# Optimization experiments

Hardware: AMD Instinct MI355X
Metric: run time of the kernel (lower is better)

The kernel has to match this reference:

```python
import jax, jax.numpy as jnp
import numpy as np

T, H, I, E, TOPK = 8192, 2048, 4096, 8, 2

def setup_inputs() -> dict:
    key = jax.random.key(0)
    k1, k2, k3, k4 = jax.random.split(key, 4)
    x = jax.random.normal(k1, (T, H), dtype=jnp.float32)
    gate_w = jax.random.normal(k2, (E, H), dtype=jnp.float32) * 0.02
    ws = jax.random.normal(k3, (E, 2 * I, H), dtype=jnp.float32) * 0.02
    w2s = jax.random.normal(k4, (E, H, I), dtype=jnp.float32) * 0.02
    return {"x": x, "gate_w": gate_w, "ws": ws, "w2s": w2s, "top_k": TOPK}

def reference(x, gate_w, ws, w2s, top_k):
    num_tokens = x.shape[0]
    num_experts = ws.shape[0]
    inter = w2s.shape[2]
    # --- router (fused_topk): softmax -> top-k -> renormalize ---
    logits = x @ gate_w.T                       # [T, E]
    probs = jax.nn.softmax(logits, axis=-1)
    topk_w, topk_ids = jax.lax.top_k(probs, top_k)   # [T, K]
    if top_k > 1:
        topk_w = topk_w / jnp.sum(topk_w, axis=-1, keepdims=True)
    # dense combine-weights [E, T]: sum of routing weights per (token, expert)
    tok = jnp.arange(num_tokens)
    cw = jnp.zeros((num_tokens, num_experts), dtype=x.dtype)
    cw = cw.at[tok[:, None], topk_ids].add(topk_w)
    cw = cw.T                                   # [E, T]
    # --- fused_experts: per-expert gated-SiLU MLP, weighted combine ---
    def body(acc, inp):
        e_ws, e_w2, e_cw = inp                  # [2I,H], [H,I], [T]
        gu = x @ e_ws.T                         # [T, 2I]
        g, u = gu[:, :inter], gu[:, inter:]
        h = jax.nn.silu(g) * u                  # SiluAndMul
        out = h @ e_w2.T                        # [T, H]
        return acc + e_cw[:, None] * out, None
    init = jnp.zeros_like(x)
    final, _ = jax.lax.scan(body, init, (ws, w2s, cw))
    return final
```

## Files before the change

### kernel.cpp

```cpp
#include <hip/hip_runtime.h>
#include <hip/hip_fp16.h>
#include <cstdint>
#include <cstddef>

#define TTOK 8192
#define HD   2048
#define ID   4096
#define NE   8
#define NPAIR (TTOK * 2)
#define PADMAX (NPAIR + NE * 128)

typedef _Float16 h8 __attribute__((ext_vector_type(8)));
typedef _Float16 h4 __attribute__((ext_vector_type(4)));
typedef float    f4 __attribute__((ext_vector_type(4)));

__device__ __forceinline__ void async_cp16(const void* g, void* l) {
  __builtin_amdgcn_global_load_lds(
      (const __attribute__((address_space(1))) unsigned int*)g,
      (__attribute__((address_space(3))) unsigned int*)l, 16, 0, 0);
}

__device__ __forceinline__ f4 zero4() { f4 z = {0.f, 0.f, 0.f, 0.f}; return z; }

__global__ void cvt_kernel(const float* __restrict__ src, _Float16* __restrict__ dst, size_t n) {
  size_t stride = (size_t)gridDim.x * blockDim.x * 8;
  for (size_t i = ((size_t)blockIdx.x * blockDim.x + threadIdx.x) * 8; i < n; i += stride) {
    const float4* s = (const float4*)(src + i);
    float4 a = s[0], b = s[1];
    h8 o;
    o[0] = (_Float16)a.x; o[1] = (_Float16)a.y; o[2] = (_Float16)a.z; o[3] = (_Float16)a.w;
    o[4] = (_Float16)b.x; o[5] = (_Float16)b.y; o[6] = (_Float16)b.z; o[7] = (_Float16)b.w;
    *(h8*)(dst + i) = o;
  }
}

__global__ __launch_bounds__(256) void gate_kernel(
    const float* __restrict__ x, const float* __restrict__ gw,
    int* __restrict__ counts, int* __restrict__ tids, float* __restrict__ tw) {
  int lane = threadIdx.x & 63;
  int t = blockIdx.x * 4 + (threadIdx.x >> 6);
  const float* xr = x + (size_t)t * HD;
  float acc[NE];
#pragma unroll
  for (int e = 0; e < NE; e++) acc[e] = 0.f;
  for (int j = lane; j < HD; j += 64) {
    float xv = xr[j];
#pragma unroll
    for (int e = 0; e < NE; e++) acc[e] += xv * gw[e * HD + j];
  }
#pragma unroll
  for (int off = 32; off > 0; off >>= 1) {
#pragma unroll
    for (int e = 0; e < NE; e++) acc[e] += __shfl_xor(acc[e], off, 64);
  }
  if (lane == 0) {
    int e0 = 0; float v0 = acc[0];
#pragma unroll
    for (int e = 1; e < NE; e++) if (acc[e] > v0) { v0 = acc[e]; e0 = e; }
    int e1 = -1; float v1 = -1e30f;
#pragma unroll
    for (int e = 0; e < NE; e++) if (e != e0 && acc[e] > v1) { v1 = acc[e]; e1 = e; }
    float b = __expf(v1 - v0);
    float w0 = 1.f / (1.f + b);
    tids[2 * t] = e0; tids[2 * t + 1] = e1;
    tw[2 * t] = w0;   tw[2 * t + 1] = b * w0;
    atomicAdd(&counts[e0], 1); atomicAdd(&counts[e1], 1);
  }
}

__global__ void scan_kernel(const int* __restrict__ counts, int* __restrict__ offs,
                            int* __restrict__ cursor) {
  if (threadIdx.x == 0 && blockIdx.x == 0) {
    int off = 0;
    for (int e = 0; e < NE; e++) {
      offs[e] = off; cursor[e] = off;
      off += ((counts[e] + 127) >> 7) << 7;
    }
    offs[NE] = off;
  }
}

__global__ void scatter_kernel(const int* __restrict__ tids, const float* __restrict__ tw,
                               int* __restrict__ cursor, int* __restrict__ perm,
                               float* __restrict__ pw) {
  int t = blockIdx.x * 256 + threadIdx.x;
#pragma unroll
  for (int k = 0; k < 2; k++) {
    int e = tids[2 * t + k];
    int pos = atomicAdd(&cursor[e], 1);
    perm[pos] = t; pw[pos] = tw[2 * t + k];
  }
}

__global__ void padfill_kernel(const int* __restrict__ counts, const int* __restrict__ offs,
                               int* __restrict__ perm) {
  int s = blockIdx.x * 256 + threadIdx.x;
#pragma unroll
  for (int e = 0; e < NE; e++) {
    if (s >= offs[e] + counts[e] && s < offs[e + 1]) perm[s] = -1;
  }
}

template <bool WPRE>
__global__ __launch_bounds__(256, 2) void gemm1_kernel(
    const _Float16* __restrict__ xh, const float* __restrict__ wsf,
    const _Float16* __restrict__ wsh,
    const int* __restrict__ counts, const int* __restrict__ offs,
    const int* __restrict__ perm, _Float16* __restrict__ hbuf) {
  int e = blockIdx.y >> 6, rb = blockIdx.y & 63;
  if (rb >= ((counts[e] + 127) >> 7)) return;
  int row0 = offs[e] + (rb << 7);
  int n0 = blockIdx.x << 7;

  __shared__ _Float16 As[128 * 32];
  __shared__ _Float16 Bg[128 * 32];
  __shared__ _Float16 Bu[128 * 32];
  int tid = threadIdx.x, lane = tid & 63, wid = tid >> 6, wr = wid >> 1, wc = wid & 1;

  const _Float16* asrc[2];
#pragma unroll
  for (int i = 0; i < 2; i++) {
    int slot = i * 256 + tid, r = slot >> 2, seg = slot & 3;
    int p = perm[row0 + r]; if (p < 0) p = 0;
    asrc[i] = xh + (size_t)p * HD + seg * 8;
  }
  const _Float16* bsg[2]; const _Float16* bsu[2];
  const float* fsg = nullptr; const float* fsu = nullptr;
  if constexpr (WPRE) {
#pragma unroll
    for (int i = 0; i < 2; i++) {
      int slot = i * 256 + tid, r = slot >> 2, seg = slot & 3;
      bsg[i] = wsh + ((size_t)e * 2 * ID + n0 + r) * HD + seg * 8;
      bsu[i] = wsh + ((size_t)e * 2 * ID + ID + n0 + r) * HD + seg * 8;
    }
  } else {
    int tr = tid >> 1, hf = tid & 1;
    fsg = wsf + ((size_t)e * 2 * ID + n0 + tr) * HD + hf * 16;
    fsu = wsf + ((size_t)e * 2 * ID + ID + n0 + tr) * HD + hf * 16;
  }

  auto stage = [&](int kt) {
    int kof = kt * 32;
#pragma unroll
    for (int i = 0; i < 2; i++) async_cp16(asrc[i] + kof, &As[(i * 256 + tid) * 8]);
    if constexpr (WPRE) {
#pragma unroll
      for (int i = 0; i < 2; i++) {
        async_cp16(bsg[i] + kof, &Bg[(i * 256 + tid) * 8]);
        async_cp16(bsu[i] + kof, &Bu[(i * 256 + tid) * 8]);
      }
    } else {
      int tr = tid >> 1, hf = tid & 1;
#pragma unroll
      for (int j = 0; j < 4; j++) {
        float4 vg = *(const float4*)(fsg + kof + j * 4);
        float4 vu = *(const float4*)(fsu + kof + j * 4);
        h4 og, ou;
        og[0] = (_Float16)vg.x; og[1] = (_Float16)vg.y; og[2] = (_Float16)vg.z; og[3] = (_Float16)vg.w;
        ou[0] = (_Float16)vu.x; ou[1] = (_Float16)vu.y; ou[2] = (_Float16)vu.z; ou[3] = (_Float16)vu.w;
        *(h4*)&Bg[tr * 32 + hf * 16 + j * 4] = og;
        *(h4*)&Bu[tr * 32 + hf * 16 + j * 4] = ou;
      }
    }
  };

  f4 accg[4][4], accu[4][4];
#pragma unroll
  for (int m = 0; m < 4; m++)
#pragma unroll
    for (int n = 0; n < 4; n++) { accg[m][n] = zero4(); accu[m][n] = zero4(); }

  stage(0);
  const int NK = HD / 32;
  for (int kt = 0; kt < NK; ++kt) {
    __syncthreads();
    int lr = lane & 15, ks = lane >> 4;
    h8 af[4], bg[4], bu[4];
#pragma unroll
    for (int m = 0; m < 4; m++)
      af[m] = *(const h8*)&As[((wr << 6) + (m << 4) + lr) * 32 + ks * 8];
#pragma unroll
    for (int n = 0; n < 4; n++) {
      bg[n] = *(const h8*)&Bg[((wc << 6) + (n << 4) + lr) * 32 + ks * 8];
      bu[n] = *(const h8*)&Bu[((wc << 6) + (n << 4) + lr) * 32 + ks * 8];
    }
#pragma unroll
    for (int m = 0; m < 4; m++)
#pragma unroll
      for (int n = 0; n < 4; n++) {
        accg[m][n] = __builtin_amdgcn_mfma_f32_16x16x32_f16(af[m], bg[n], accg[m][n], 0, 0, 0);
        accu[m][n] = __builtin_amdgcn_mfma_f32_16x16x32_f16(af[m], bu[n], accu[m][n], 0, 0, 0);
      }
    __syncthreads();
    if (kt + 1 < NK) stage(kt + 1);
  }

  int lr = lane & 15, lg = lane >> 4;
#pragma unroll
  for (int m = 0; m < 4; m++)
#pragma unroll
    for (int n = 0; n < 4; n++)
#pragma unroll
      for (int r = 0; r < 4; r++) {
        int grow = (wr << 6) + (m << 4) + (lg << 2) + r;
        int gcol = n0 + (wc << 6) + (n << 4) + lr;
        float g = accg[m][n][r], u = accu[m][n][r];
        float hv = g / (1.f + __expf(-g)) * u;
        hbuf[(size_t)(row0 + grow) * ID + gcol] = (_Float16)hv;
      }
}

template <bool WPRE>
__global__ __launch_bounds__(256, 2) void gemm2_kernel(
    const _Float16* __restrict__ hbuf, const float* __restrict__ w2f,
    const _Float16* __restrict__ w2h,
    const int* __restrict__ counts, const int* __restrict__ offs,
    const int* __restrict__ perm, const float* __restrict__ pw,
    float* __restrict__ out) {
  int e = blockIdx.y >> 6, rb = blockIdx.y & 63;
  if (rb >= ((counts[e] + 127) >> 7)) return;
  int row0 = offs[e] + (rb << 7);
  int n0 = blockIdx.x << 7;

  __shared__ _Float16 As[128 * 32];
  __shared__ _Float16 Bs[128 * 32];
  int tid = threadIdx.x, lane = tid & 63, wid = tid >> 6, wr = wid >> 1, wc = wid & 1;

  const _Float16* asrc[2]; const _Float16* bs[2]; const float* fs = nullptr;
#pragma unroll
  for (int i = 0; i < 2; i++) {
    int slot = i * 256 + tid, r = slot >> 2, seg = slot & 3;
    asrc[i] = hbuf + (size_t)(row0 + r) * ID + seg * 8;
    if constexpr (WPRE) bs[i] = w2h + ((size_t)e * HD + n0 + r) * ID + seg * 8;
  }
  if constexpr (!WPRE) {
    int tr = tid >> 1, hf = tid & 1;
    fs = w2f + ((size_t)e * HD + n0 + tr) * ID + hf * 16;
  }

  auto stage = [&](int kt) {
    int kof = kt * 32;
#pragma unroll
    for (int i = 0; i < 2; i++) async_cp16(asrc[i] + kof, &As[(i * 256 + tid) * 8]);
    if constexpr (WPRE) {
#pragma unroll
      for (int i = 0; i < 2; i++) async_cp16(bs[i] + kof, &Bs[(i * 256 + tid) * 8]);
    } else {
      int tr = tid >> 1, hf = tid & 1;
#pragma unroll
      for (int j = 0; j < 4; j++) {
        float4 v = *(const float4*)(fs + kof + j * 4);
        h4 o;
        o[0] = (_Float16)v.x; o[1] = (_Float16)v.y; o[2] = (_Float16)v.z; o[3] = (_Float16)v.w;
        *(h4*)&Bs[tr * 32 + hf * 16 + j * 4] = o;
      }
    }
  };

  f4 acc[4][4];
#pragma unroll
  for (int m = 0; m < 4; m++)
#pragma unroll
    for (int n = 0; n < 4; n++) acc[m][n] = zero4();

  stage(0);
  const int NK = ID / 32;
  for (int kt = 0; kt < NK; ++kt) {
    __syncthreads();
    int lr = lane & 15, ks = lane >> 4;
    h8 af[4], bf[4];
#pragma unroll
    for (int m = 0; m < 4; m++)
      af[m] = *(const h8*)&As[((wr << 6) + (m << 4) + lr) * 32 + ks * 8];
#pragma unroll
    for (int n = 0; n < 4; n++)
      bf[n] = *(const h8*)&Bs[((wc << 6) + (n << 4) + lr) * 32 + ks * 8];
#pragma unroll
    for (int m = 0; m < 4; m++)
#pragma unroll
      for (int n = 0; n < 4; n++)
        acc[m][n] = __builtin_amdgcn_mfma_f32_16x16x32_f16(af[m], bf[n], acc[m][n], 0, 0, 0);
    __syncthreads();
    if (kt + 1 < NK) stage(kt + 1);
  }

  int lr = lane & 15, lg = lane >> 4;
#pragma unroll
  for (int m = 0; m < 4; m++)
#pragma unroll
    for (int r = 0; r < 4; r++) {
      int row = row0 + (wr << 6) + (m << 4) + (lg << 2) + r;
      int t = perm[row];
      if (t < 0) continue;
      float w = pw[row];
#pragma unroll
      for (int n = 0; n < 4; n++) {
        int gcol = n0 + (wc << 6) + (n << 4) + lr;
        atomicAdd(&out[(size_t)t * HD + gcol], acc[m][n][r] * w);
      }
    }
}

extern "C" void kernel_launch(void* const* d_in, const int* in_sizes, int n_in,
                              void* d_out, int out_size, void* d_ws, size_t ws_size,
                              hipStream_t stream) {
  const float* x   = (const float*)d_in[0];
  const float* gw  = (const float*)d_in[1];
  const float* wsf = (const float*)d_in[2];
  const float* w2f = (const float*)d_in[3];

  int* counts  = (int*)d_ws;
  int* offs    = counts + 8;
  int* cursor  = offs + 16;
  int* tids    = cursor + 8;
  float* tw    = (float*)(tids + NPAIR);
  int* perm    = (int*)(tw + NPAIR);
  float* pw    = (float*)(perm + PADMAX);

  char* base = (char*)d_ws;
  size_t off_xh = (size_t)512 * 1024;
  size_t off_h  = off_xh + (size_t)TTOK * HD * 2;
  size_t base_end = off_h + (size_t)PADMAX * ID * 2;
  if (ws_size < base_end) return;

  _Float16* xh = (_Float16*)(base + off_xh);
  _Float16* hb = (_Float16*)(base + off_h);

  size_t nws = (size_t)NE * 2 * ID * HD;
  size_t nw2 = (size_t)NE * HD * ID;
  bool wpre = (ws_size >= base_end + (nws + nw2) * 2);
  _Float16* wsh = nullptr; _Float16* w2h = nullptr;
  if (wpre) { wsh = (_Float16*)(base + base_end); w2h = wsh + nws; }

  hipMemsetAsync(counts, 0, 64, stream);
  hipMemsetAsync(d_out, 0, (size_t)out_size * 4, stream);

  cvt_kernel<<<2048, 256, 0, stream>>>(x, xh, (size_t)TTOK * HD);
  if (wpre) {
    cvt_kernel<<<4096, 256, 0, stream>>>(wsf, wsh, nws);
    cvt_kernel<<<4096, 256, 0, stream>>>(w2f, w2h, nw2);
  }
  gate_kernel<<<TTOK / 4, 256, 0, stream>>>(x, gw, counts, tids, tw);
  scan_kernel<<<1, 64, 0, stream>>>(counts, offs, cursor);
  scatter_kernel<<<TTOK / 256, 256, 0, stream>>>(tids, tw, cursor, perm, pw);
  padfill_kernel<<<PADMAX / 256, 256, 0, stream>>>(counts, offs, perm);

  dim3 g1(ID / 128, NE * (TTOK / 128));
  dim3 g2(HD / 128, NE * (TTOK / 128));
  if (wpre) {
    gemm1_kernel<true><<<g1, 256, 0, stream>>>(xh, wsf, wsh, counts, offs, perm, hb);
    gemm2_kernel<true><<<g2, 256, 0, stream>>>(hb, w2f, w2h, counts, offs, perm, pw, (float*)d_out);
  } else {
    gemm1_kernel<false><<<g1, 256, 0, stream>>>(xh, wsf, wsh, counts, offs, perm, hb);
    gemm2_kernel<false><<<g2, 256, 0, stream>>>(hb, w2f, w2h, counts, offs, perm, pw, (float*)d_out);
  }
}
```

Measured before the change: 1.626 ms.

## Rewrite MoE GEMMs with 256-row tiles, 4-stage async pipeline, swizzled LDS

Both expert GEMMs are rewritten to use 512-thread blocks with 256-row tiles. Expert padding grows to 256 rows, and a 4-buffer global_load_lds pipeline uses explicit vmcnt waits, raw barriers and an XOR-swizzled shared-memory layout. gemm1 now reads fp32 activations directly and converts them in registers, which drops the separate x conversion pass. Block IDs are remapped for locality, setprio is raised around the MFMA loops, and the fp32-weight fallback path is removed. The intent is to hide load latency, cut LDS bank conflicts and improve operand reuse, at the cost of more padding rows, a fixed large workspace requirement and 128 KB of shared memory per block.

```diff
diff --git a/kernel.cpp b/kernel.cpp
--- a/kernel.cpp
+++ b/kernel.cpp
@@ -8,11 +8,14 @@
 #define ID   4096
 #define NE   8
 #define NPAIR (TTOK * 2)
-#define PADMAX (NPAIR + NE * 128)
+#define PADROWS (NPAIR + NE * 256)
 
 typedef _Float16 h8 __attribute__((ext_vector_type(8)));
-typedef _Float16 h4 __attribute__((ext_vector_type(4)));
 typedef float    f4 __attribute__((ext_vector_type(4)));
+
+#define VMWAIT(n) asm volatile("s_waitcnt vmcnt(" #n ")" ::: "memory")
+#define LGKMWAIT0 asm volatile("s_waitcnt lgkmcnt(0)" ::: "memory")
+#define MEMFENCE  asm volatile("" ::: "memory")
 
 __device__ __forceinline__ void async_cp16(const void* g, void* l) {
   __builtin_amdgcn_global_load_lds(
@@ -74,7 +77,7 @@
     int off = 0;
     for (int e = 0; e < NE; e++) {
       offs[e] = off; cursor[e] = off;
-      off += ((counts[e] + 127) >> 7) << 7;
+      off += ((counts[e] + 255) >> 8) << 8;
     }
     offs[NE] = off;
   }
@@ -101,204 +104,210 @@
   }
 }
 
-template <bool WPRE>
-__global__ __launch_bounds__(256, 2) void gemm1_kernel(
-    const _Float16* __restrict__ xh, const float* __restrict__ wsf,
-    const _Float16* __restrict__ wsh,
+__global__ __launch_bounds__(512, 2) void gemm1_kernel(
+    const float* __restrict__ x, const _Float16* __restrict__ wsh,
     const int* __restrict__ counts, const int* __restrict__ offs,
     const int* __restrict__ perm, _Float16* __restrict__ hbuf) {
-  int e = blockIdx.y >> 6, rb = blockIdx.y & 63;
-  if (rb >= ((counts[e] + 127) >> 7)) return;
-  int row0 = offs[e] + (rb << 7);
-  int n0 = blockIdx.x << 7;
-
-  __shared__ _Float16 As[128 * 32];
-  __shared__ _Float16 Bg[128 * 32];
-  __shared__ _Float16 Bu[128 * 32];
-  int tid = threadIdx.x, lane = tid & 63, wid = tid >> 6, wr = wid >> 1, wc = wid & 1;
-
-  const _Float16* asrc[2];
-#pragma unroll
-  for (int i = 0; i < 2; i++) {
-    int slot = i * 256 + tid, r = slot >> 2, seg = slot & 3;
-    int p = perm[row0 + r]; if (p < 0) p = 0;
-    asrc[i] = xh + (size_t)p * HD + seg * 8;
-  }
-  const _Float16* bsg[2]; const _Float16* bsu[2];
-  const float* fsg = nullptr; const float* fsu = nullptr;
-  if constexpr (WPRE) {
-#pragma unroll
-    for (int i = 0; i < 2; i++) {
-      int slot = i * 256 + tid, r = slot >> 2, seg = slot & 3;
-      bsg[i] = wsh + ((size_t)e * 2 * ID + n0 + r) * HD + seg * 8;
-      bsu[i] = wsh + ((size_t)e * 2 * ID + ID + n0 + r) * HD + seg * 8;
+  int lin = blockIdx.x + gridDim.x * blockIdx.y;
+  int wg = (lin & 7) * 1024 + (lin >> 3);
+  int bx = wg & 31;
+  int by = wg >> 5;
+  int e = by >> 5, rb = by & 31;
+  if (rb >= ((counts[e] + 255) >> 8)) return;
+  int row0 = offs[e] + (rb << 8);
+  int n0 = bx << 7;
+
+  __shared__ _Float16 smem[65536];
+  int tid = threadIdx.x;
+  int lane = tid & 63, wid = tid >> 6, wr = wid >> 2, wc = wid & 3;
+  int lr = lane & 15, kc = lane >> 4;
+  int ach = kc ^ ((lr >> 1) & 3);
+
+  int ar = tid >> 1, ahf = tid & 1;
+  int pa = perm[row0 + ar]; if (pa < 0) pa = 0;
+  const float* aptr = x + (size_t)pa * HD + ahf * 16;
+  int as = (ar >> 1) & 3;
+  int aw0 = ar * 32 + (((ahf << 1) ^ as) << 3);
+  int aw1 = ar * 32 + ((((ahf << 1) | 1) ^ as) << 3);
+
+  int br = tid >> 2;
+  int swzc = (tid & 3) ^ ((tid >> 3) & 3);
+  const _Float16* bptr0 = wsh + ((size_t)e * 2 * ID + (n0 + br)) * HD + swzc * 8;
+  const _Float16* bptr1 = wsh + ((size_t)e * 2 * ID + ID + (n0 + br)) * HD + swzc * 8;
+
+  f4 acc[8][4];
+#pragma unroll
+  for (int m = 0; m < 8; m++)
+#pragma unroll
+    for (int n = 0; n < 4; n++) acc[m][n] = zero4();
+
+  float4 fP0, fP1, fP2, fP3, fN0, fN1, fN2, fN3;
+
+  auto stageB = [&](int kt, int b) {
+    async_cp16(bptr0 + kt * 32, &smem[b * 16384 + 8192 + tid * 8]);
+    async_cp16(bptr1 + kt * 32, &smem[b * 16384 + 8192 + 4096 + tid * 8]);
+  };
+  auto writeA = [&](int b) {
+    h8 o0, o1;
+    o0[0]=(_Float16)fP0.x; o0[1]=(_Float16)fP0.y; o0[2]=(_Float16)fP0.z; o0[3]=(_Float16)fP0.w;
+    o0[4]=(_Float16)fP1.x; o0[5]=(_Float16)fP1.y; o0[6]=(_Float16)fP1.z; o0[7]=(_Float16)fP1.w;
+    o1[0]=(_Float16)fP2.x; o1[1]=(_Float16)fP2.y; o1[2]=(_Float16)fP2.z; o1[3]=(_Float16)fP2.w;
+    o1[4]=(_Float16)fP3.x; o1[5]=(_Float16)fP3.y; o1[6]=(_Float16)fP3.z; o1[7]=(_Float16)fP3.w;
+    *(h8*)&smem[b * 16384 + aw0] = o0;
+    *(h8*)&smem[b * 16384 + aw1] = o1;
+  };
+  auto compute = [&](int b) {
+    int abase = b * 16384, bbase = b * 16384 + 8192;
+    h8 af[8], bf[4];
+#pragma unroll
+    for (int m = 0; m < 8; m++)
+      af[m] = *(const h8*)&smem[abase + (wr * 128 + m * 16 + lr) * 32 + ach * 8];
+#pragma unroll
+    for (int n = 0; n < 4; n++) {
+      int rB = (n < 2) ? (wc * 32 + n * 16 + lr) : (128 + wc * 32 + (n - 2) * 16 + lr);
+      bf[n] = *(const h8*)&smem[bbase + rB * 32 + ach * 8];
     }
-  } else {
-    int tr = tid >> 1, hf = tid & 1;
-    fsg = wsf + ((size_t)e * 2 * ID + n0 + tr) * HD + hf * 16;
-    fsu = wsf + ((size_t)e * 2 * ID + ID + n0 + tr) * HD + hf * 16;
-  }
-
-  auto stage = [&](int kt) {
-    int kof = kt * 32;
-#pragma unroll
-    for (int i = 0; i < 2; i++) async_cp16(asrc[i] + kof, &As[(i * 256 + tid) * 8]);
-    if constexpr (WPRE) {
-#pragma unroll
-      for (int i = 0; i < 2; i++) {
-        async_cp16(bsg[i] + kof, &Bg[(i * 256 + tid) * 8]);
-        async_cp16(bsu[i] + kof, &Bu[(i * 256 + tid) * 8]);
+    __builtin_amdgcn_s_setprio(1);
+#pragma unroll
+    for (int m = 0; m < 8; m++)
+#pragma unroll
+      for (int n = 0; n < 4; n++)
+        acc[m][n] = __builtin_amdgcn_mfma_f32_16x16x32_f16(af[m], bf[n], acc[m][n], 0, 0, 0);
+    __builtin_amdgcn_s_setprio(0);
+  };
+
+#pragma unroll
+  for (int t = 0; t < 3; t++) {
+    const float4* p = (const float4*)(aptr + t * 32);
+    fP0 = p[0]; fP1 = p[1]; fP2 = p[2]; fP3 = p[3];
+    stageB(t, t);
+    writeA(t);
+  }
+  {
+    const float4* p = (const float4*)(aptr + 3 * 32);
+    fP0 = p[0]; fP1 = p[1]; fP2 = p[2]; fP3 = p[3];
+  }
+  LGKMWAIT0;
+
+  const int NK = HD / 32;
+  for (int k = 0; k <= NK - 4; ++k) {
+    int b = k & 3, tb = (k + 3) & 3;
+    VMWAIT(8);
+    __builtin_amdgcn_s_barrier();
+    MEMFENCE;
+    if (k + 4 < NK) {
+      const float4* p = (const float4*)(aptr + (k + 4) * 32);
+      fN0 = p[0]; fN1 = p[1]; fN2 = p[2]; fN3 = p[3];
+    }
+    stageB(k + 3, tb);
+    writeA(tb);
+    compute(b);
+    fP0 = fN0; fP1 = fN1; fP2 = fN2; fP3 = fN3;
+  }
+  VMWAIT(2); __builtin_amdgcn_s_barrier(); MEMFENCE; compute((NK - 3) & 3);
+  VMWAIT(2); __builtin_amdgcn_s_barrier(); MEMFENCE; compute((NK - 2) & 3);
+  VMWAIT(0); __builtin_amdgcn_s_barrier(); MEMFENCE; compute((NK - 1) & 3);
+
+  int hr0 = row0 + wr * 128 + kc * 4;
+  int hc0 = n0 + wc * 32 + lr;
+#pragma unroll
+  for (int m = 0; m < 8; m++)
+#pragma unroll
+    for (int n = 0; n < 2; n++)
+#pragma unroll
+      for (int r = 0; r < 4; r++) {
+        float g = acc[m][n][r], u = acc[m][n + 2][r];
+        float hv = g / (1.f + __expf(-g)) * u;
+        hbuf[(size_t)(hr0 + m * 16 + r) * ID + hc0 + n * 16] = (_Float16)hv;
       }
-    } else {
-      int tr = tid >> 1, hf = tid & 1;
-#pragma unroll
-      for (int j = 0; j < 4; j++) {
-        float4 vg = *(const float4*)(fsg + kof + j * 4);
-        float4 vu = *(const float4*)(fsu + kof + j * 4);
-        h4 og, ou;
-        og[0] = (_Float16)vg.x; og[1] = (_Float16)vg.y; og[2] = (_Float16)vg.z; og[3] = (_Float16)vg.w;
-        ou[0] = (_Float16)vu.x; ou[1] = (_Float16)vu.y; ou[2] = (_Float16)vu.z; ou[3] = (_Float16)vu.w;
-        *(h4*)&Bg[tr * 32 + hf * 16 + j * 4] = og;
-        *(h4*)&Bu[tr * 32 + hf * 16 + j * 4] = ou;
-      }
-    }
-  };
-
-  f4 accg[4][4], accu[4][4];
-#pragma unroll
-  for (int m = 0; m < 4; m++)
-#pragma unroll
-    for (int n = 0; n < 4; n++) { accg[m][n] = zero4(); accu[m][n] = zero4(); }
-
-  stage(0);
-  const int NK = HD / 32;
-  for (int kt = 0; kt < NK; ++kt) {
-    __syncthreads();
-    int lr = lane & 15, ks = lane >> 4;
-    h8 af[4], bg[4], bu[4];
-#pragma unroll
-    for (int m = 0; m < 4; m++)
-      af[m] = *(const h8*)&As[((wr << 6) + (m << 4) + lr) * 32 + ks * 8];
-#pragma unroll
-    for (int n = 0; n < 4; n++) {
-      bg[n] = *(const h8*)&Bg[((wc << 6) + (n << 4) + lr) * 32 + ks * 8];
-      bu[n] = *(const h8*)&Bu[((wc << 6) + (n << 4) + lr) * 32 + ks * 8];
-    }
-#pragma unroll
-    for (int m = 0; m < 4; m++)
-#pragma unroll
-      for (int n = 0; n < 4; n++) {
-        accg[m][n] = __builtin_amdgcn_mfma_f32_16x16x32_f16(af[m], bg[n], accg[m][n], 0, 0, 0);
-        accu[m][n] = __builtin_amdgcn_mfma_f32_16x16x32_f16(af[m], bu[n], accu[m][n], 0, 0, 0);
-      }
-    __syncthreads();
-    if (kt + 1 < NK) stage(kt + 1);
-  }
-
-  int lr = lane & 15, lg = lane >> 4;
-#pragma unroll
-  for (int m = 0; m < 4; m++)
-#pragma unroll
-    for (int n = 0; n < 4; n++)
-#pragma unroll
-      for (int r = 0; r < 4; r++) {
-        int grow = (wr << 6) + (m << 4) + (lg << 2) + r;
-        int gcol = n0 + (wc << 6) + (n << 4) + lr;
-        float g = accg[m][n][r], u = accu[m][n][r];
-        float hv = g / (1.f + __expf(-g)) * u;
-        hbuf[(size_t)(row0 + grow) * ID + gcol] = (_Float16)hv;
-      }
-}
-
-template <bool WPRE>
-__global__ __launch_bounds__(256, 2) void gemm2_kernel(
-    const _Float16* __restrict__ hbuf, const float* __restrict__ w2f,
-    const _Float16* __restrict__ w2h,
+}
+
+__global__ __launch_bounds__(512, 2) void gemm2_kernel(
+    const _Float16* __restrict__ hbuf, const _Float16* __restrict__ w2h,
     const int* __restrict__ counts, const int* __restrict__ offs,
     const int* __restrict__ perm, const float* __restrict__ pw,
     float* __restrict__ out) {
-  int e = blockIdx.y >> 6, rb = blockIdx.y & 63;
-  if (rb >= ((counts[e] + 127) >> 7)) return;
-  int row0 = offs[e] + (rb << 7);
-  int n0 = blockIdx.x << 7;
-
-  __shared__ _Float16 As[128 * 32];
-  __shared__ _Float16 Bs[128 * 32];
-  int tid = threadIdx.x, lane = tid & 63, wid = tid >> 6, wr = wid >> 1, wc = wid & 1;
-
-  const _Float16* asrc[2]; const _Float16* bs[2]; const float* fs = nullptr;
-#pragma unroll
-  for (int i = 0; i < 2; i++) {
-    int slot = i * 256 + tid, r = slot >> 2, seg = slot & 3;
-    asrc[i] = hbuf + (size_t)(row0 + r) * ID + seg * 8;
-    if constexpr (WPRE) bs[i] = w2h + ((size_t)e * HD + n0 + r) * ID + seg * 8;
-  }
-  if constexpr (!WPRE) {
-    int tr = tid >> 1, hf = tid & 1;
-    fs = w2f + ((size_t)e * HD + n0 + tr) * ID + hf * 16;
-  }
-
-  auto stage = [&](int kt) {
-    int kof = kt * 32;
-#pragma unroll
-    for (int i = 0; i < 2; i++) async_cp16(asrc[i] + kof, &As[(i * 256 + tid) * 8]);
-    if constexpr (WPRE) {
-#pragma unroll
-      for (int i = 0; i < 2; i++) async_cp16(bs[i] + kof, &Bs[(i * 256 + tid) * 8]);
-    } else {
-      int tr = tid >> 1, hf = tid & 1;
-#pragma unroll
-      for (int j = 0; j < 4; j++) {
-        float4 v = *(const float4*)(fs + kof + j * 4);
-        h4 o;
-        o[0] = (_Float16)v.x; o[1] = (_Float16)v.y; o[2] = (_Float16)v.z; o[3] = (_Float16)v.w;
-        *(h4*)&Bs[tr * 32 + hf * 16 + j * 4] = o;
-      }
-    }
-  };
-
-  f4 acc[4][4];
-#pragma unroll
-  for (int m = 0; m < 4; m++)
+  int lin = blockIdx.x + gridDim.x * blockIdx.y;
+  int wg = (lin & 7) * 256 + (lin >> 3);
+  int bx = wg & 7;
+  int by = wg >> 3;
+  int e = by >> 5, rb = by & 31;
+  if (rb >= ((counts[e] + 255) >> 8)) return;
+  int row0 = offs[e] + (rb << 8);
+  int n0 = bx << 8;
+
+  __shared__ _Float16 smem[65536];
+  int tid = threadIdx.x;
+  int lane = tid & 63, wid = tid >> 6, wr = wid >> 2, wc = wid & 3;
+  int lr = lane & 15, kc = lane >> 4;
+  int ach = kc ^ ((lr >> 1) & 3);
+
+  int br = tid >> 2;
+  int swzc = (tid & 3) ^ ((tid >> 3) & 3);
+  const _Float16* aptr0 = hbuf + (size_t)(row0 + br) * ID + swzc * 8;
+  const _Float16* aptr1 = hbuf + (size_t)(row0 + 128 + br) * ID + swzc * 8;
+  const _Float16* bptr0 = w2h + ((size_t)e * HD + n0 + br) * ID + swzc * 8;
+  const _Float16* bptr1 = w2h + ((size_t)e * HD + n0 + 128 + br) * ID + swzc * 8;
+
+  f4 acc[8][4];
+#pragma unroll
+  for (int m = 0; m < 8; m++)
 #pragma unroll
     for (int n = 0; n < 4; n++) acc[m][n] = zero4();
 
-  stage(0);
-  const int NK = ID / 32;
-  for (int kt = 0; kt < NK; ++kt) {
-    __syncthreads();
-    int lr = lane & 15, ks = lane >> 4;
-    h8 af[4], bf[4];
-#pragma unroll
-    for (int m = 0; m < 4; m++)
-      af[m] = *(const h8*)&As[((wr << 6) + (m << 4) + lr) * 32 + ks * 8];
+  auto stage = [&](int kt, int b) {
+    async_cp16(aptr0 + kt * 32, &smem[b * 16384 + tid * 8]);
+    async_cp16(aptr1 + kt * 32, &smem[b * 16384 + 4096 + tid * 8]);
+    async_cp16(bptr0 + kt * 32, &smem[b * 16384 + 8192 + tid * 8]);
+    async_cp16(bptr1 + kt * 32, &smem[b * 16384 + 8192 + 4096 + tid * 8]);
+  };
+  auto compute = [&](int b) {
+    int abase = b * 16384, bbase = b * 16384 + 8192;
+    h8 af[8], bf[4];
+#pragma unroll
+    for (int m = 0; m < 8; m++)
+      af[m] = *(const h8*)&smem[abase + (wr * 128 + m * 16 + lr) * 32 + ach * 8];
 #pragma unroll
     for (int n = 0; n < 4; n++)
-      bf[n] = *(const h8*)&Bs[((wc << 6) + (n << 4) + lr) * 32 + ks * 8];
-#pragma unroll
-    for (int m = 0; m < 4; m++)
+      bf[n] = *(const h8*)&smem[bbase + (wc * 64 + n * 16 + lr) * 32 + ach * 8];
+    __builtin_amdgcn_s_setprio(1);
+#pragma unroll
+    for (int m = 0; m < 8; m++)
 #pragma unroll
       for (int n = 0; n < 4; n++)
         acc[m][n] = __builtin_amdgcn_mfma_f32_16x16x32_f16(af[m], bf[n], acc[m][n], 0, 0, 0);
-    __syncthreads();
-    if (kt + 1 < NK) stage(kt + 1);
-  }
-
-  int lr = lane & 15, lg = lane >> 4;
-#pragma unroll
-  for (int m = 0; m < 4; m++)
+    __builtin_amdgcn_s_setprio(0);
+  };
+
+  stage(0, 0); stage(1, 1); stage(2, 2);
+
+  const int NK = ID / 32;
+  for (int k = 0; k <= NK - 4; ++k) {
+    int b = k & 3, tb = (k + 3) & 3;
+    VMWAIT(8);
+    __builtin_amdgcn_s_barrier();
+    MEMFENCE;
+    stage(k + 3, tb);
+    compute(b);
+  }
+  VMWAIT(8); __builtin_amdgcn_s_barrier(); MEMFENCE; compute((NK - 3) & 3);
+  VMWAIT(4); __builtin_amdgcn_s_barrier(); MEMFENCE; compute((NK - 2) & 3);
+  VMWAIT(0); __builtin_amdgcn_s_barrier(); MEMFENCE; compute((NK - 1) & 3);
+
+#pragma unroll
+  for (int m = 0; m < 8; m++) {
 #pragma unroll
     for (int r = 0; r < 4; r++) {
-      int row = row0 + (wr << 6) + (m << 4) + (lg << 2) + r;
+      int row = row0 + wr * 128 + m * 16 + kc * 4 + r;
       int t = perm[row];
       if (t < 0) continue;
       float w = pw[row];
-#pragma unroll
-      for (int n = 0; n < 4; n++) {
-        int gcol = n0 + (wc << 6) + (n << 4) + lr;
-        atomicAdd(&out[(size_t)t * HD + gcol], acc[m][n][r] * w);
-      }
+      float* orow = out + (size_t)t * HD + n0 + wc * 64 + lr;
+#pragma unroll
+      for (int n = 0; n < 4; n++)
+        atomicAdd(orow + n * 16, acc[m][n][r] * w);
     }
+  }
 }
 
 extern "C" void kernel_launch(void* const* d_in, const int* in_sizes, int n_in,
@@ -315,43 +324,34 @@
   int* tids    = cursor + 8;
   float* tw    = (float*)(tids + NPAIR);
   int* perm    = (int*)(tw + NPAIR);
-  float* pw    = (float*)(perm + PADMAX);
+  float* pw    = (float*)(perm + PADROWS);
 
   char* base = (char*)d_ws;
-  size_t off_xh = (size_t)512 * 1024;
-  size_t off_h  = off_xh + (size_t)TTOK * HD * 2;
-  size_t base_end = off_h + (size_t)PADMAX * ID * 2;
-  if (ws_size < base_end) return;
-
-  _Float16* xh = (_Float16*)(base + off_xh);
-  _Float16* hb = (_Float16*)(base + off_h);
+  size_t off_h   = (size_t)512 * 1024;
+  size_t off_wsh = off_h + (size_t)PADROWS * ID * 2;
+  size_t off_w2h = off_wsh + (size_t)NE * 2 * ID * HD * 2;
+  size_t need    = off_w2h + (size_t)NE * HD * ID * 2;
+  if (ws_size < need) return;
+
+  _Float16* hb  = (_Float16*)(base + off_h);
+  _Float16* wsh = (_Float16*)(base + off_wsh);
+  _Float16* w2h = (_Float16*)(base + off_w2h);
 
   size_t nws = (size_t)NE * 2 * ID * HD;
   size_t nw2 = (size_t)NE * HD * ID;
-  bool wpre = (ws_size >= base_end + (nws + nw2) * 2);
-  _Float16* wsh = nullptr; _Float16* w2h = nullptr;
-  if (wpre) { wsh = (_Float16*)(base + base_end); w2h = wsh + nws; }
 
   hipMemsetAsync(counts, 0, 64, stream);
   hipMemsetAsync(d_out, 0, (size_t)out_size * 4, stream);
 
-  cvt_kernel<<<2048, 256, 0, stream>>>(x, xh, (size_t)TTOK * HD);
-  if (wpre) {
-    cvt_kernel<<<4096, 256, 0, stream>>>(wsf, wsh, nws);
-    cvt_kernel<<<4096, 256, 0, stream>>>(w2f, w2h, nw2);
-  }
+  cvt_kernel<<<4096, 256, 0, stream>>>(wsf, wsh, nws);
+  cvt_kernel<<<4096, 256, 0, stream>>>(w2f, w2h, nw2);
   gate_kernel<<<TTOK / 4, 256, 0, stream>>>(x, gw, counts, tids, tw);
   scan_kernel<<<1, 64, 0, stream>>>(counts, offs, cursor);
   scatter_kernel<<<TTOK / 256, 256, 0, stream>>>(tids, tw, cursor, perm, pw);
-  padfill_kernel<<<PADMAX / 256, 256, 0, stream>>>(counts, offs, perm);
-
-  dim3 g1(ID / 128, NE * (TTOK / 128));
-  dim3 g2(HD / 128, NE * (TTOK / 128));
-  if (wpre) {
-    gemm1_kernel<true><<<g1, 256, 0, stream>>>(xh, wsf, wsh, counts, offs, perm, hb);
-    gemm2_kernel<true><<<g2, 256, 0, stream>>>(hb, w2f, w2h, counts, offs, perm, pw, (float*)d_out);
-  } else {
-    gemm1_kernel<false><<<g1, 256, 0, stream>>>(xh, wsf, wsh, counts, offs, perm, hb);
-    gemm2_kernel<false><<<g2, 256, 0, stream>>>(hb, w2f, w2h, counts, offs, perm, pw, (float*)d_out);
-  }
-}
+  padfill_kernel<<<PADROWS / 256, 256, 0, stream>>>(counts, offs, perm);
+
+  gemm1_kernel<<<dim3(ID / 128, NE * (TTOK / 256)), 512, 0, stream>>>(
+      x, wsh, counts, offs, perm, hb);
+  gemm2_kernel<<<dim3(HD / 256, NE * (TTOK / 256)), 512, 0, stream>>>(
+      hb, w2h, counts, offs, perm, pw, (float*)d_out);
+}
```

After: 1.900 ms. 16.8% more time.
